# Optimization experiments

Hardware: AMD Instinct MI355X
Metric: run time of the kernel (lower is better)

## Reference

```python
import jax, jax.numpy as jnp
import numpy as np

B, T = 128, 512
V, E, U, K = 50000, 100, 128, 32


def _lstm(x, Wk, Wr, b):
    # x: [B, T, D] -> [B, T, U], Keras LSTM gate order i,f,g,o
    Bd = x.shape[0]
    Ud = Wr.shape[0]
    xs = jnp.swapaxes(x, 0, 1)  # [T, B, D]

    def step(carry, xt):
        h, c = carry
        z = xt @ Wk + h @ Wr + b
        i, f, g, o = jnp.split(z, 4, axis=-1)
        c = jax.nn.sigmoid(f) * c + jax.nn.sigmoid(i) * jnp.tanh(g)
        h = jax.nn.sigmoid(o) * jnp.tanh(c)
        return (h, c), h

    init = (jnp.zeros((Bd, Ud), x.dtype), jnp.zeros((Bd, Ud), x.dtype))
    _, hs = jax.lax.scan(step, init, xs)
    return jnp.swapaxes(hs, 0, 1)


def _crf_logZ(em, trans):
    # em: [B, T, K] emissions; trans: [K, K]. Forward algorithm log-partition.
    alpha0 = em[:, 0]  # [B, K]
    es = jnp.swapaxes(em[:, 1:], 0, 1)  # [T-1, B, K]

    def step(alpha, et):
        # alpha[b, i] + trans[i, j] -> logsumexp over i, plus emission
        alpha = jax.nn.logsumexp(alpha[:, :, None] + trans[None], axis=1) + et
        return alpha, None

    alphaT, _ = jax.lax.scan(step, alpha0, es)
    return jax.nn.logsumexp(alphaT, axis=-1)  # [B]


def setup_inputs() -> dict:
    key = jax.random.key(0)
    ks = jax.random.split(key, 11)
    s = 0.1
    return {
        "tokens": jax.random.randint(ks[0], (B, T), 0, V, dtype=jnp.int32),
        "emb": jax.random.normal(ks[1], (V, E), jnp.float32) * s,
        "Wk_f": jax.random.normal(ks[2], (E, 4 * U), jnp.float32) * s,
        "Wr_f": jax.random.normal(ks[3], (U, 4 * U), jnp.float32) * s,
        "b_f": jnp.zeros((4 * U,), jnp.float32),
        "Wk_b": jax.random.normal(ks[4], (E, 4 * U), jnp.float32) * s,
        "Wr_b": jax.random.normal(ks[5], (U, 4 * U), jnp.float32) * s,
        "b_b": jnp.zeros((4 * U,), jnp.float32),
        "crf_kernel": jax.random.normal(ks[6], (2 * U, K), jnp.float32) * s,
        "crf_bias": jnp.zeros((K,), jnp.float32),
        "trans": jax.random.normal(ks[7], (K, K), jnp.float32) * s,
    }


def reference(tokens, emb, Wk_f, Wr_f, b_f, Wk_b, Wr_b, b_b, crf_kernel, crf_bias, trans):
    x = emb[tokens]  # [B, T, E]
    h_f = _lstm(x, Wk_f, Wr_f, b_f)
    h_b = _lstm(x[:, ::-1], Wk_b, Wr_b, b_b)[:, ::-1]
    h = jnp.concatenate([h_f, h_b], axis=-1)  # [B, T, 2U] (dropout = identity at inference)
    em = h @ crf_kernel + crf_bias  # [B, T, K] CRF emission potentials
    return _crf_logZ(em, trans)  # [B] log-partition via CRF forward DP
```

## Files before the change

### kernel.cpp

```cpp
#include <hip/hip_runtime.h>
#include <hip/hip_bf16.h>

#define B_  128
#define T_  512
#define V_  50000
#define VP  50016
#define E_  100
#define U_  128
#define K_  32
#define G4  512
#define KP  128

typedef _Float16 h2_t __attribute__((ext_vector_type(2)));
typedef _Float16 f16x8 __attribute__((ext_vector_type(8)));
typedef __fp16   h2raw_t __attribute__((ext_vector_type(2)));
typedef short    bf16x8 __attribute__((ext_vector_type(8)));
typedef float    f32x4  __attribute__((ext_vector_type(4)));

__device__ __forceinline__ h2_t pk2(float a, float b) {
    h2raw_t r = __builtin_amdgcn_cvt_pkrtz(a, b);
    union { h2raw_t r; h2_t h; } u; u.r = r; return u.h;
}

#if __has_builtin(__builtin_amdgcn_rcpf)
__device__ __forceinline__ float rcp_f(float x) { return __builtin_amdgcn_rcpf(x); }
#else
__device__ __forceinline__ float rcp_f(float x) { return 1.f / x; }
#endif

__device__ __forceinline__ unsigned short bf16_bits(float v) {
    __hip_bfloat16 b = __float2bfloat16(v);
    union { __hip_bfloat16 b; unsigned short s; } u; u.b = b; return u.s;
}
__device__ __forceinline__ float bf2f(unsigned short u) {
    union { unsigned int i; float f; } x; x.i = ((unsigned int)u) << 16; return x.f;
}

__global__ __launch_bounds__(128) void pack_b_kernel(
    const float* __restrict__ Wk_f, const float* __restrict__ Wk_b,
    __hip_bfloat16* __restrict__ Bb)
{
    const int n = blockIdx.x;
    const int k = threadIdx.x;
    float v = 0.f;
    if (k < E_) v = (n < 512) ? Wk_f[k * 512 + n] : Wk_b[k * 512 + (n - 512)];
    Bb[n * KP + k] = __float2bfloat16(v);
}

__global__ __launch_bounds__(256, 2) void proj_mfma_kernel(
    const float* __restrict__ emb,
    const __hip_bfloat16* __restrict__ Bb,
    const float* __restrict__ b_f, const float* __restrict__ b_b,
    __hip_bfloat16* __restrict__ proj)
{
    const int r0   = blockIdx.x * 32;
    const int tid  = threadIdx.x;
    const int wv   = tid >> 6;
    const int lane = tid & 63;
    const int quad = lane >> 4;
    const int l16  = lane & 15;

    __shared__ __align__(16) float C_lds[32][268];
    unsigned short* A_st = (unsigned short*)&C_lds[0][0];

    for (int idx = tid; idx < 32 * 64; idx += 256) {
        int r = idx >> 6, kk = idx & 63;
        int vr = r0 + r; if (vr >= V_) vr = V_ - 1;
        unsigned int w = 0;
        if (kk < 50) {
            float2 v = *(const float2*)(emb + (long long)vr * E_ + 2 * kk);
            w = ((unsigned int)bf16_bits(v.y) << 16) | bf16_bits(v.x);
        }
        *(unsigned int*)&A_st[r * 136 + 2 * kk] = w;
    }
    __syncthreads();

    bf16x8 af[2][4];
    #pragma unroll
    for (int mt = 0; mt < 2; ++mt)
        #pragma unroll
        for (int kc = 0; kc < 4; ++kc)
            af[mt][kc] = *(const bf16x8*)&A_st[(mt * 16 + l16) * 136 +
                                               kc * 32 + quad * 8];
    __syncthreads();

    const unsigned short* Bu = (const unsigned short*)Bb;

    for (int ng = 0; ng < 4; ++ng) {
        const int n0 = ng * 256;

        bf16x8 bfr[4][4];
        #pragma unroll
        for (int nt = 0; nt < 4; ++nt)
            #pragma unroll
            for (int kc = 0; kc < 4; ++kc)
                bfr[nt][kc] = *(const bf16x8*)(Bu +
                    (n0 + wv * 64 + nt * 16 + l16) * KP + kc * 32 + quad * 8);

        f32x4 acc[2][4];
        #pragma unroll
        for (int mt = 0; mt < 2; ++mt)
            #pragma unroll
            for (int nt = 0; nt < 4; ++nt)
                acc[mt][nt] = (f32x4){0.f, 0.f, 0.f, 0.f};

        #pragma unroll
        for (int mt = 0; mt < 2; ++mt)
            #pragma unroll
            for (int nt = 0; nt < 4; ++nt)
                #pragma unroll
                for (int kc = 0; kc < 4; ++kc)
                    acc[mt][nt] = __builtin_amdgcn_mfma_f32_16x16x32_bf16(
                        af[mt][kc], bfr[nt][kc], acc[mt][nt], 0, 0, 0);

        #pragma unroll
        for (int mt = 0; mt < 2; ++mt)
            #pragma unroll
            for (int nt = 0; nt < 4; ++nt)
                #pragma unroll
                for (int v = 0; v < 4; ++v)
                    C_lds[mt * 16 + quad * 4 + v][wv * 64 + nt * 16 + l16] =
                        acc[mt][nt][v];
        __syncthreads();

        const float* bias = (n0 < 512) ? b_f : b_b;
        const int nbase = n0 & 511;
        for (int idx = tid; idx < 32 * 128; idx += 256) {
            int r = idx >> 7, cc = (idx & 127) * 2;
            float v0 = C_lds[r][cc]     + bias[nbase + cc];
            float v1 = C_lds[r][cc + 1] + bias[nbase + cc + 1];
            unsigned int w = ((unsigned int)bf16_bits(v1) << 16) | bf16_bits(v0);
            *(unsigned int*)(proj + (long long)(r0 + r) * 1024 + n0 + cc) = w;
        }
        __syncthreads();
    }
}

__device__ __forceinline__ float sigmoid_f(float x) {
    return rcp_f(1.f + __expf(-x));
}
__device__ __forceinline__ float tanh_f(float x) {
    return 1.f - 2.f * rcp_f(__expf(2.f * x) + 1.f);
}

__global__ __launch_bounds__(512, 1) void lstm_kernel(
    const __hip_bfloat16* __restrict__ proj,
    const int* __restrict__ tokens,
    const float* __restrict__ Wr_f, const float* __restrict__ Wr_b,
    __hip_bfloat16* __restrict__ h_buf)
{
    const int bid  = blockIdx.x;
    const int dir  = bid >> 5;
    const int b0   = (bid & 31) * 4;
    const int tid  = threadIdx.x;
    const int w    = tid >> 6;
    const int lane = tid & 63;
    const int quad = lane >> 4;
    const int l16  = lane & 15;
    const int unit = 16 * w + l16;

    const float* Wr = dir ? Wr_b : Wr_f;

    union uf16 { f16x8 v; h2_t p[4]; };
    f16x8 wb[4][4];
    #pragma unroll
    for (int gq = 0; gq < 4; ++gq) {
        const int col = gq * 128 + unit;
        #pragma unroll
        for (int kc = 0; kc < 4; ++kc) {
            const int k0 = kc * 32 + quad * 8;
            uf16 u;
            #pragma unroll
            for (int jj = 0; jj < 4; ++jj)
                u.p[jj] = pk2(Wr[(k0 + 2 * jj)     * G4 + col],
                              Wr[(k0 + 2 * jj + 1) * G4 + col]);
            wb[gq][kc] = u.v;
        }
    }

    __shared__ __align__(16) _Float16      h_lds[2][4][144];
    __shared__ __align__(16) unsigned short xkb[2][4][520];
    __shared__ unsigned short tok_lds[4][512];

    for (int idx = tid; idx < 4 * 512; idx += 512) {
        int chain = idx >> 9, tt = idx & 511;
        int tsrc = dir ? (T_ - 1 - tt) : tt;
        tok_lds[chain][tt] = (unsigned short)tokens[(b0 + chain) * T_ + tsrc];
    }
    for (int idx = tid; idx < 4 * 144; idx += 512)
        ((_Float16*)h_lds[0])[idx] = (_Float16)0.f;
    __syncthreads();

    const int sc = tid >> 7;
    const int sj = tid & 127;
    const unsigned short* prbase = (const unsigned short*)proj + dir * 512;

    int v[4][2];
    #pragma unroll
    for (int d = 0; d < 4; ++d) {
        int tk = tok_lds[sc][d];
        const unsigned int* p32 = (const unsigned int*)(prbase + (size_t)tk * 1024);
        v[d][0] = p32[sj];
        v[d][1] = p32[sj + 128];
    }
    *(unsigned int*)&xkb[0][sc][2 * sj]       = v[0][0];
    *(unsigned int*)&xkb[0][sc][2 * sj + 256] = v[0][1];
    __syncthreads();

    float c = 0.f;

    for (int t4 = 0; t4 < T_ / 4; ++t4) {
        #pragma unroll
        for (int u = 0; u < 4; ++u) {
            const int t  = t4 * 4 + u;
            const int cb = u & 1, nb = cb ^ 1;

            f16x8 a[4];
            #pragma unroll
            for (int kc = 0; kc < 4; ++kc)
                a[kc] = *(const f16x8*)&h_lds[cb][l16 >> 2][kc * 32 + quad * 8];
            unsigned short xk[4];
            #pragma unroll
            for (int gq = 0; gq < 4; ++gq)
                xk[gq] = xkb[cb][quad][gq * 128 + unit];

            {
                int tnx = t + 4; if (tnx > T_ - 1) tnx = T_ - 1;
                int tk = tok_lds[sc][tnx];
                const unsigned int* p32 =
                    (const unsigned int*)(prbase + (size_t)tk * 1024);
                v[u][0] = p32[sj];
                v[u][1] = p32[sj + 128];
            }

            f32x4 acc[4];
            #pragma unroll
            for (int gq = 0; gq < 4; ++gq)
                acc[gq] = (f32x4){0.f, 0.f, 0.f, 0.f};
            #pragma unroll
            for (int gq = 0; gq < 4; ++gq)
                #pragma unroll
                for (int kc = 0; kc < 4; ++kc)
                    acc[gq] = __builtin_amdgcn_mfma_f32_16x16x32_f16(
                        a[kc], wb[gq][kc], acc[gq], 0, 0, 0);

            float zi = acc[0][0] + bf2f(xk[0]);
            float zf = acc[1][0] + bf2f(xk[1]);
            float zg = acc[2][0] + bf2f(xk[2]);
            float zo = acc[3][0] + bf2f(xk[3]);
            c = sigmoid_f(zf) * c + sigmoid_f(zi) * tanh_f(zg);
            float h = sigmoid_f(zo) * tanh_f(c);
            h_lds[nb][quad][unit] = (_Float16)h;

            const int ttime = dir ? (T_ - 1 - t) : t;
            h_buf[((size_t)(b0 + quad) * T_ + ttime) * 256 + dir * 128 + unit] =
                __float2bfloat16(h);

            {
                const int pw = (u + 1) & 3;
                *(unsigned int*)&xkb[nb][sc][2 * sj]       = v[pw][0];
                *(unsigned int*)&xkb[nb][sc][2 * sj + 256] = v[pw][1];
            }

            asm volatile("s_waitcnt lgkmcnt(0)" ::: "memory");
            __builtin_amdgcn_s_barrier();
            asm volatile("" ::: "memory");
        }
    }
}

__global__ __launch_bounds__(256) void em_kernel(
    const __hip_bfloat16* __restrict__ h_buf,
    const float* __restrict__ ck, const float* __restrict__ cb,
    float* __restrict__ em)
{
    const int tid  = threadIdx.x;
    const int part = tid >> 5;
    const int k    = tid & 31;

    float ckr[32];
    #pragma unroll
    for (int i = 0; i < 32; ++i)
        ckr[i] = ck[(part * 32 + i) * K_ + k];
    const float cbk = cb[k];

    __shared__ float h_l[8][256];
    __shared__ float part_l[8][8][K_];

    const int r0 = blockIdx.x * 64;

    for (int round = 0; round < 8; ++round) {
        const int rbase = r0 + round * 8;
        #pragma unroll
        for (int j = 0; j < 8; ++j)
            h_l[j][tid] = __bfloat162float(h_buf[(long long)(rbase + j) * 256 + tid]);
        __syncthreads();

        #pragma unroll
        for (int j = 0; j < 8; ++j) {
            float pp = 0.f;
            #pragma unroll
            for (int i = 0; i < 32; ++i)
                pp = fmaf(h_l[j][part * 32 + i], ckr[i], pp);
            part_l[j][part][k] = pp;
        }
        __syncthreads();

        {
            int j2 = tid >> 5;
            float e = cbk;
            #pragma unroll
            for (int pq = 0; pq < 8; ++pq) e += part_l[j2][pq][k];
            em[(long long)(rbase + j2) * K_ + k] = e;
        }
        __syncthreads();
    }
}

#define PF_ 8
__global__ __launch_bounds__(64) void crf_kernel(
    const float* __restrict__ em,
    const float* __restrict__ trans,
    float* __restrict__ out)
{
    const int b    = blockIdx.x;
    const int lane = threadIdx.x;
    const int k    = lane & 31;
    const int half = lane >> 5;

    float etr[16];
    #pragma unroll
    for (int i = 0; i < 16; ++i)
        etr[i] = __expf(trans[(half * 16 + i) * K_ + k]);

    const float* em_b = em + (long long)b * T_ * K_;

    float ep[PF_];
    #pragma unroll
    for (int d = 0; d < PF_; ++d)
        ep[d] = em_b[d * K_ + k];

    float w = 0.f;
    float L = 0.f;
    for (int tb = 0; tb < T_; tb += PF_) {
        float en[PF_];
        if (tb + PF_ < T_) {
            #pragma unroll
            for (int d = 0; d < PF_; ++d)
                en[d] = em_b[(tb + PF_ + d) * K_ + k];
        } else {
            #pragma unroll
            for (int d = 0; d < PF_; ++d) en[d] = 0.f;
        }

        float eem[PF_];
        #pragma unroll
        for (int d = 0; d < PF_; ++d) eem[d] = __expf(ep[d]);

        #pragma unroll
        for (int d = 0; d < PF_; ++d) {
            if (tb + d == 0) {
                w = eem[d];
            } else {
                float acc = 0.f;
                #pragma unroll
                for (int i = 0; i < 16; ++i) {
                    float wv = __shfl(w, half * 16 + i, 64);
                    acc = fmaf(wv, etr[i], acc);
                }
                acc += __shfl_xor(acc, 32, 64);
                w = acc * eem[d];
            }
        }

        {
            float w0 = __shfl(w, 0, 64);
            w *= rcp_f(w0);
            L += __logf(w0);
        }

        #pragma unroll
        for (int d = 0; d < PF_; ++d) ep[d] = en[d];
    }

    float s = w;
    #pragma unroll
    for (int d = 1; d < 32; d <<= 1)
        s += __shfl_xor(s, d, 64);
    if (lane == 0) out[b] = L + __logf(s);
}

extern "C" void kernel_launch(void* const* d_in, const int* in_sizes, int n_in,
                              void* d_out, int out_size, void* d_ws, size_t ws_size,
                              hipStream_t stream)
{
    const int*   tokens = (const int*)  d_in[0];
    const float* emb    = (const float*)d_in[1];
    const float* Wk_f   = (const float*)d_in[2];
    const float* Wr_f   = (const float*)d_in[3];
    const float* b_f    = (const float*)d_in[4];
    const float* Wk_b   = (const float*)d_in[5];
    const float* Wr_b   = (const float*)d_in[6];
    const float* b_b    = (const float*)d_in[7];
    const float* ck     = (const float*)d_in[8];
    const float* cb     = (const float*)d_in[9];
    const float* trans  = (const float*)d_in[10];
    float* out = (float*)d_out;

    const long long ROWS = (long long)B_ * T_;
    __hip_bfloat16* proj  = (__hip_bfloat16*)d_ws;
    __hip_bfloat16* h_buf = proj + (long long)VP * 1024;
    float* em = (float*)(h_buf + ROWS * 256);
    __hip_bfloat16* Bb = (__hip_bfloat16*)(em + ROWS * K_);

    hipLaunchKernelGGL(pack_b_kernel, dim3(1024), dim3(128), 0, stream,
                       Wk_f, Wk_b, Bb);
    hipLaunchKernelGGL(proj_mfma_kernel, dim3(VP / 32), dim3(256), 0, stream,
                       emb, Bb, b_f, b_b, proj);
    hipLaunchKernelGGL(lstm_kernel, dim3(64), dim3(512), 0, stream,
                       proj, tokens, Wr_f, Wr_b, h_buf);
    hipLaunchKernelGGL(em_kernel, dim3((int)(ROWS / 64)), dim3(256), 0, stream,
                       h_buf, ck, cb, em);
    hipLaunchKernelGGL(crf_kernel, dim3(B_), dim3(64), 0, stream,
                       em, trans, out);
}
```

Before: 529.2 us.

## Prefetch LSTM input projections directly into registers and enlarge projection tiles

The LSTM recurrence no longer stages the precomputed input projections through a double-buffered LDS array. Each lane now loads its own four gate values for the token four steps ahead straight into registers. This removes an LDS write/read pair per step, at the cost of scattered 2-byte global loads. Separately, the vocab projection GEMM now runs 64-row tiles with 512 threads per block, so each loaded B fragment is reused across twice as many rows. Writes past the last padded row are clamped to the final row.

```diff
diff --git a/kernel.cpp b/kernel.cpp
--- a/kernel.cpp
+++ b/kernel.cpp
@@ -47,23 +47,25 @@
     Bb[n * KP + k] = __float2bfloat16(v);
 }
 
-__global__ __launch_bounds__(256, 2) void proj_mfma_kernel(
+__global__ __launch_bounds__(512, 1) void proj_mfma_kernel(
     const float* __restrict__ emb,
     const __hip_bfloat16* __restrict__ Bb,
     const float* __restrict__ b_f, const float* __restrict__ b_b,
     __hip_bfloat16* __restrict__ proj)
 {
-    const int r0   = blockIdx.x * 32;
+    const int r0   = blockIdx.x * 64;
     const int tid  = threadIdx.x;
     const int wv   = tid >> 6;
     const int lane = tid & 63;
     const int quad = lane >> 4;
     const int l16  = lane & 15;
-
-    __shared__ __align__(16) float C_lds[32][268];
+    const int mh   = wv >> 2;
+    const int cg   = wv & 3;
+
+    __shared__ __align__(16) float C_lds[64][268];
     unsigned short* A_st = (unsigned short*)&C_lds[0][0];
 
-    for (int idx = tid; idx < 32 * 64; idx += 256) {
+    for (int idx = tid; idx < 64 * 64; idx += 512) {
         int r = idx >> 6, kk = idx & 63;
         int vr = r0 + r; if (vr >= V_) vr = V_ - 1;
         unsigned int w = 0;
@@ -80,7 +82,7 @@
     for (int mt = 0; mt < 2; ++mt)
         #pragma unroll
         for (int kc = 0; kc < 4; ++kc)
-            af[mt][kc] = *(const bf16x8*)&A_st[(mt * 16 + l16) * 136 +
+            af[mt][kc] = *(const bf16x8*)&A_st[(mh * 32 + mt * 16 + l16) * 136 +
                                                kc * 32 + quad * 8];
     __syncthreads();
 
@@ -95,7 +97,7 @@
             #pragma unroll
             for (int kc = 0; kc < 4; ++kc)
                 bfr[nt][kc] = *(const bf16x8*)(Bu +
-                    (n0 + wv * 64 + nt * 16 + l16) * KP + kc * 32 + quad * 8);
+                    (n0 + cg * 64 + nt * 16 + l16) * KP + kc * 32 + quad * 8);
 
         f32x4 acc[2][4];
         #pragma unroll
@@ -119,18 +121,19 @@
             for (int nt = 0; nt < 4; ++nt)
                 #pragma unroll
                 for (int v = 0; v < 4; ++v)
-                    C_lds[mt * 16 + quad * 4 + v][wv * 64 + nt * 16 + l16] =
-                        acc[mt][nt][v];
+                    C_lds[mh * 32 + mt * 16 + quad * 4 + v]
+                         [cg * 64 + nt * 16 + l16] = acc[mt][nt][v];
         __syncthreads();
 
         const float* bias = (n0 < 512) ? b_f : b_b;
         const int nbase = n0 & 511;
-        for (int idx = tid; idx < 32 * 128; idx += 256) {
+        for (int idx = tid; idx < 64 * 128; idx += 512) {
             int r = idx >> 7, cc = (idx & 127) * 2;
             float v0 = C_lds[r][cc]     + bias[nbase + cc];
             float v1 = C_lds[r][cc + 1] + bias[nbase + cc + 1];
             unsigned int w = ((unsigned int)bf16_bits(v1) << 16) | bf16_bits(v0);
-            *(unsigned int*)(proj + (long long)(r0 + r) * 1024 + n0 + cc) = w;
+            int row = r0 + r; if (row >= VP) row = VP - 1;
+            *(unsigned int*)(proj + (long long)row * 1024 + n0 + cc) = w;
         }
         __syncthreads();
     }
@@ -178,8 +181,7 @@
         }
     }
 
-    __shared__ __align__(16) _Float16      h_lds[2][4][144];
-    __shared__ __align__(16) unsigned short xkb[2][4][520];
+    __shared__ __align__(16) _Float16 h_lds[2][4][144];
     __shared__ unsigned short tok_lds[4][512];
 
     for (int idx = tid; idx < 4 * 512; idx += 512) {
@@ -191,21 +193,18 @@
         ((_Float16*)h_lds[0])[idx] = (_Float16)0.f;
     __syncthreads();
 
-    const int sc = tid >> 7;
-    const int sj = tid & 127;
-    const unsigned short* prbase = (const unsigned short*)proj + dir * 512;
-
-    int v[4][2];
+    const unsigned short* prl = (const unsigned short*)proj + dir * 512 + unit;
+
+    unsigned short xq[4][4];
     #pragma unroll
     for (int d = 0; d < 4; ++d) {
-        int tk = tok_lds[sc][d];
-        const unsigned int* p32 = (const unsigned int*)(prbase + (size_t)tk * 1024);
-        v[d][0] = p32[sj];
-        v[d][1] = p32[sj + 128];
-    }
-    *(unsigned int*)&xkb[0][sc][2 * sj]       = v[0][0];
-    *(unsigned int*)&xkb[0][sc][2 * sj + 256] = v[0][1];
-    __syncthreads();
+        int tk = tok_lds[quad][d];
+        const unsigned short* pr = prl + (size_t)tk * 1024;
+        xq[d][0] = pr[0];
+        xq[d][1] = pr[128];
+        xq[d][2] = pr[256];
+        xq[d][3] = pr[384];
+    }
 
     float c = 0.f;
 
@@ -215,22 +214,24 @@
             const int t  = t4 * 4 + u;
             const int cb = u & 1, nb = cb ^ 1;
 
+            float xv0 = bf2f(xq[u][0]);
+            float xv1 = bf2f(xq[u][1]);
+            float xv2 = bf2f(xq[u][2]);
+            float xv3 = bf2f(xq[u][3]);
+
             f16x8 a[4];
             #pragma unroll
             for (int kc = 0; kc < 4; ++kc)
                 a[kc] = *(const f16x8*)&h_lds[cb][l16 >> 2][kc * 32 + quad * 8];
-            unsigned short xk[4];
-            #pragma unroll
-            for (int gq = 0; gq < 4; ++gq)
-                xk[gq] = xkb[cb][quad][gq * 128 + unit];
 
             {
                 int tnx = t + 4; if (tnx > T_ - 1) tnx = T_ - 1;
-                int tk = tok_lds[sc][tnx];
-                const unsigned int* p32 =
-                    (const unsigned int*)(prbase + (size_t)tk * 1024);
-                v[u][0] = p32[sj];
-                v[u][1] = p32[sj + 128];
+                int tk = tok_lds[quad][tnx];
+                const unsigned short* pr = prl + (size_t)tk * 1024;
+                xq[u][0] = pr[0];
+                xq[u][1] = pr[128];
+                xq[u][2] = pr[256];
+                xq[u][3] = pr[384];
             }
 
             f32x4 acc[4];
@@ -244,10 +245,10 @@
                     acc[gq] = __builtin_amdgcn_mfma_f32_16x16x32_f16(
                         a[kc], wb[gq][kc], acc[gq], 0, 0, 0);
 
-            float zi = acc[0][0] + bf2f(xk[0]);
-            float zf = acc[1][0] + bf2f(xk[1]);
-            float zg = acc[2][0] + bf2f(xk[2]);
-            float zo = acc[3][0] + bf2f(xk[3]);
+            float zi = acc[0][0] + xv0;
+            float zf = acc[1][0] + xv1;
+            float zg = acc[2][0] + xv2;
+            float zo = acc[3][0] + xv3;
             c = sigmoid_f(zf) * c + sigmoid_f(zi) * tanh_f(zg);
             float h = sigmoid_f(zo) * tanh_f(c);
             h_lds[nb][quad][unit] = (_Float16)h;
@@ -255,12 +256,6 @@
             const int ttime = dir ? (T_ - 1 - t) : t;
             h_buf[((size_t)(b0 + quad) * T_ + ttime) * 256 + dir * 128 + unit] =
                 __float2bfloat16(h);
-
-            {
-                const int pw = (u + 1) & 3;
-                *(unsigned int*)&xkb[nb][sc][2 * sj]       = v[pw][0];
-                *(unsigned int*)&xkb[nb][sc][2 * sj + 256] = v[pw][1];
-            }
 
             asm volatile("s_waitcnt lgkmcnt(0)" ::: "memory");
             __builtin_amdgcn_s_barrier();
@@ -415,7 +410,7 @@
 
     hipLaunchKernelGGL(pack_b_kernel, dim3(1024), dim3(128), 0, stream,
                        Wk_f, Wk_b, Bb);
-    hipLaunchKernelGGL(proj_mfma_kernel, dim3(VP / 32), dim3(256), 0, stream,
+    hipLaunchKernelGGL(proj_mfma_kernel, dim3((VP + 63) / 64), dim3(512), 0, stream,
                        emb, Bb, b_f, b_b, proj);
     hipLaunchKernelGGL(lstm_kernel, dim3(64), dim3(512), 0, stream,
                        proj, tokens, Wr_f, Wr_b, h_buf);
```

New measurement: 546.4 us. +3.2%, slower.
